# Kernel tuning notes

Measured on AMD Instinct MI355X. Metric: run time of the kernel, lower is better.

Reference implementation:

```python
import jax, jax.numpy as jnp
import numpy as np

KSIZE = 3  # module init kwarg


def setup_inputs() -> dict:
    key = jax.random.key(0)
    k1, k2, k3 = jax.random.split(key, 3)
    shape = (16, 3, 512, 512)  # [B, C, H, W]
    return {
        "sr": jax.random.normal(k1, shape, jnp.float32),
        "sr_ema": jax.random.normal(k2, shape, jnp.float32),
        "hr": jax.random.normal(k3, shape, jnp.float32),
    }


def _local_var(res, ksize):
    """Unbiased variance over a ksize x ksize sliding window with reflect pad.

    Matches torch: reflect-pad then unfold + var(unbiased=True). Implemented as a
    box-filter over sum and sum-of-squares (no ksize^2-larger unfold tensor).
    res: [B, 1, H, W] -> [B, 1, H, W]
    """
    pad = (ksize - 1) // 2
    rp = jnp.pad(res, ((0, 0), (0, 0), (pad, pad), (pad, pad)), mode="reflect")
    n = ksize * ksize
    win = (1, 1, ksize, ksize)
    strides = (1, 1, 1, 1)
    zero = jnp.zeros((), rp.dtype)
    s = jax.lax.reduce_window(rp, zero, jax.lax.add, win, strides, "VALID")
    sq = jax.lax.reduce_window(rp * rp, zero, jax.lax.add, win, strides, "VALID")
    # unbiased: (sum(x^2) - sum(x)^2/n) / (n-1)
    return (sq - s * s / n) / (n - 1)


def reference(sr, sr_ema, hr):
    # per-pixel channel-summed residuals, [B, 1, H, W]
    residual_ema = jnp.sum(jnp.abs(hr - sr_ema), axis=1, keepdims=True) / 255.0
    residual_sr = jnp.sum(jnp.abs(hr - sr), axis=1, keepdims=True) / 255.0

    r_det = jax.lax.stop_gradient(residual_sr)  # .clone().detach() in torch

    # patch-level weight: unbiased var over (C=1, H, W) per sample, ** (1/5)
    n_patch = r_det.shape[1] * r_det.shape[2] * r_det.shape[3]
    mean = jnp.mean(r_det, axis=(-1, -2, -3), keepdims=True)
    patch_var = jnp.sum((r_det - mean) ** 2, axis=(-1, -2, -3), keepdims=True) / (n_patch - 1)
    patch_w = patch_var ** 0.2  # [B,1,1,1]

    pixel_w = _local_var(r_det, KSIZE)  # [B,1,H,W]

    overall_w = patch_w * pixel_w
    overall_w = jnp.where(residual_sr < residual_ema, jnp.zeros((), overall_w.dtype), overall_w)

    # L1 loss (mean reduction) between weighted sr and weighted hr
    return jnp.mean(jnp.abs(overall_w * sr - overall_w * hr))
```

## Files before the change

kernel.cpp:

```cpp
#include <hip/hip_runtime.h>
#include <math.h>


#define BB 16
#define HH 512
#define WW 512
#define HW (HH * WW)
#define CHW (3 * HW)
#define BLOCKS_PER_BATCH 1024
#define NBLOCKS (BB * BLOCKS_PER_BATCH)

__global__ __launch_bounds__(256) void wl1_main(
    const float* __restrict__ sr, const float* __restrict__ srema,
    const float* __restrict__ hr,
    float* __restrict__ p_sum, float* __restrict__ p_sum2,
    float* __restrict__ p_loss) {
  __shared__ float rt[6][66];
  const int bid = blockIdx.x;
  const int b = bid >> 10;
  const int t = bid & 1023;
  const int h0 = (t >> 3) << 2;
  const int w0 = (t & 7) << 6;
  const int tid = threadIdx.x;
  const float* __restrict__ srb = sr + (size_t)b * CHW;
  const float* __restrict__ hrb = hr + (size_t)b * CHW;

  for (int idx = tid; idx < 6 * 66; idx += 256) {
    int row = idx / 66;
    int col = idx - row * 66;
    int gh = h0 - 1 + row;
    gh = gh < 0 ? -gh : gh;
    gh = gh >= HH ? 2 * HH - 2 - gh : gh;
    int gw = w0 - 1 + col;
    gw = gw < 0 ? -gw : gw;
    gw = gw >= WW ? 2 * WW - 2 - gw : gw;
    int base = gh * WW + gw;
    float s = fabsf(hrb[base] - srb[base]) +
              fabsf(hrb[base + HW] - srb[base + HW]) +
              fabsf(hrb[base + 2 * HW] - srb[base + 2 * HW]);
    rt[row][col] = s / 255.0f;
  }
  __syncthreads();

  const int lw = tid & 63, lh = tid >> 6;
  float s = 0.f, sq = 0.f;
#pragma unroll
  for (int dr = 0; dr < 3; ++dr)
#pragma unroll
    for (int dc = 0; dc < 3; ++dc) {
      float v = rt[lh + dr][lw + dc];
      s += v;
      sq += v * v;
    }
  float pvar = (sq - s * s / 9.0f) / 8.0f;
  float rc = rt[lh + 1][lw + 1];

  const int h = h0 + lh, w = w0 + lw;
  const int base = h * WW + w;
  const float* __restrict__ eb = srema + (size_t)b * CHW;
  float e = (fabsf(hrb[base] - eb[base]) +
             fabsf(hrb[base + HW] - eb[base + HW]) +
             fabsf(hrb[base + 2 * HW] - eb[base + 2 * HW])) /
            255.0f;

  float contrib = (rc < e) ? 0.0f : pvar * (255.0f * rc);

  float v1 = rc, v2 = rc * rc, v3 = contrib;
#pragma unroll
  for (int off = 32; off > 0; off >>= 1) {
    v1 += __shfl_down(v1, off, 64);
    v2 += __shfl_down(v2, off, 64);
    v3 += __shfl_down(v3, off, 64);
  }
  __shared__ float red[3][4];
  const int wave = tid >> 6, lane = tid & 63;
  if (lane == 0) {
    red[0][wave] = v1;
    red[1][wave] = v2;
    red[2][wave] = v3;
  }
  __syncthreads();
  if (tid == 0) {
    p_sum[bid] = red[0][0] + red[0][1] + red[0][2] + red[0][3];
    p_sum2[bid] = red[1][0] + red[1][1] + red[1][2] + red[1][3];
    p_loss[bid] = red[2][0] + red[2][1] + red[2][2] + red[2][3];
  }
}

__global__ __launch_bounds__(256) void wl1_batch(
    const float* __restrict__ p_sum, const float* __restrict__ p_sum2,
    const float* __restrict__ p_loss, double* __restrict__ lossb) {
  const int b = blockIdx.x, tid = threadIdx.x;
  double s = 0.0, s2 = 0.0, sl = 0.0;
  for (int k = tid; k < BLOCKS_PER_BATCH; k += 256) {
    int i = b * BLOCKS_PER_BATCH + k;
    s += (double)p_sum[i];
    s2 += (double)p_sum2[i];
    sl += (double)p_loss[i];
  }
#pragma unroll
  for (int off = 32; off > 0; off >>= 1) {
    s += __shfl_down(s, off, 64);
    s2 += __shfl_down(s2, off, 64);
    sl += __shfl_down(sl, off, 64);
  }
  __shared__ double red[3][4];
  const int wave = tid >> 6, lane = tid & 63;
  if (lane == 0) {
    red[0][wave] = s;
    red[1][wave] = s2;
    red[2][wave] = sl;
  }
  __syncthreads();
  if (tid == 0) {
    double S = red[0][0] + red[0][1] + red[0][2] + red[0][3];
    double S2 = red[1][0] + red[1][1] + red[1][2] + red[1][3];
    double SL = red[2][0] + red[2][1] + red[2][2] + red[2][3];
    const double n = (double)HW;
    double var = (S2 - S * S / n) / (n - 1.0);
    double pw = pow(var, 0.2);
    lossb[b] = pw * SL;
  }
}

__global__ void wl1_final(const double* __restrict__ lossb,
                          float* __restrict__ out) {
  const int tid = threadIdx.x;
  double v = (tid < BB) ? lossb[tid] : 0.0;
#pragma unroll
  for (int off = 32; off > 0; off >>= 1) v += __shfl_down(v, off, 64);
  if (tid == 0) out[0] = (float)(v / (double)(BB * 3 * HW));
}

extern "C" void kernel_launch(void* const* d_in, const int* in_sizes, int n_in,
                              void* d_out, int out_size, void* d_ws,
                              size_t ws_size, hipStream_t stream) {
  const float* sr = (const float*)d_in[0];
  const float* srema = (const float*)d_in[1];
  const float* hr = (const float*)d_in[2];
  float* out = (float*)d_out;

  float* p_sum = (float*)d_ws;
  float* p_sum2 = p_sum + NBLOCKS;
  float* p_loss = p_sum2 + NBLOCKS;
  double* lossb = (double*)((char*)d_ws + (size_t)3 * NBLOCKS * sizeof(float));

  wl1_main<<<NBLOCKS, 256, 0, stream>>>(sr, srema, hr, p_sum, p_sum2, p_loss);
  wl1_batch<<<BB, 256, 0, stream>>>(p_sum, p_sum2, p_loss, lossb);
  wl1_final<<<1, 64, 0, stream>>>(lossb, out);
}
```

Measured before the change: 164.7 us.

## Enlarge tiles to 16x256 with float4 loads and merge final reductions

Result: faster. 159.0 us (-3.4%).

```diff
diff --git a/kernel.cpp b/kernel.cpp
--- a/kernel.cpp
+++ b/kernel.cpp
@@ -7,65 +7,115 @@
 #define WW 512
 #define HW (HH * WW)
 #define CHW (3 * HW)
-#define BLOCKS_PER_BATCH 1024
-#define NBLOCKS (BB * BLOCKS_PER_BATCH)
+#define TILES_PER_BATCH 64
+#define NBLOCKS (BB * TILES_PER_BATCH)
+#define LDS_STRIDE 264
+
+__device__ __forceinline__ int reflect_h(int gh) {
+  gh = gh < 0 ? -gh : gh;
+  return gh >= HH ? 2 * HH - 2 - gh : gh;
+}
 
 __global__ __launch_bounds__(256) void wl1_main(
     const float* __restrict__ sr, const float* __restrict__ srema,
     const float* __restrict__ hr,
     float* __restrict__ p_sum, float* __restrict__ p_sum2,
     float* __restrict__ p_loss) {
-  __shared__ float rt[6][66];
+  __shared__ float rt[18][LDS_STRIDE];
   const int bid = blockIdx.x;
-  const int b = bid >> 10;
-  const int t = bid & 1023;
-  const int h0 = (t >> 3) << 2;
-  const int w0 = (t & 7) << 6;
+  const int b = bid >> 6;
+  const int t = bid & 63;
+  const int h0 = (t >> 1) << 4;
+  const int w0 = (t & 1) << 8;
   const int tid = threadIdx.x;
+  const int c4 = tid & 63;
+  const int rs = tid >> 6;
   const float* __restrict__ srb = sr + (size_t)b * CHW;
   const float* __restrict__ hrb = hr + (size_t)b * CHW;
+  const float* __restrict__ eb = srema + (size_t)b * CHW;
 
-  for (int idx = tid; idx < 6 * 66; idx += 256) {
-    int row = idx / 66;
-    int col = idx - row * 66;
-    int gh = h0 - 1 + row;
-    gh = gh < 0 ? -gh : gh;
-    gh = gh >= HH ? 2 * HH - 2 - gh : gh;
-    int gw = w0 - 1 + col;
-    gw = gw < 0 ? -gw : gw;
-    gw = gw >= WW ? 2 * WW - 2 - gw : gw;
+#pragma unroll
+  for (int it = 0; it < 5; ++it) {
+    int row = it * 4 + rs;
+    if (row < 18) {
+      int gh = reflect_h(h0 - 1 + row);
+      const float* hb = hrb + gh * WW + w0 + 4 * c4;
+      const float* sb = srb + gh * WW + w0 + 4 * c4;
+      float4 ha = *(const float4*)(hb);
+      float4 hbv = *(const float4*)(hb + HW);
+      float4 hc = *(const float4*)(hb + 2 * HW);
+      float4 sa = *(const float4*)(sb);
+      float4 sbv = *(const float4*)(sb + HW);
+      float4 sc = *(const float4*)(sb + 2 * HW);
+      float4 r4;
+      r4.x = (fabsf(ha.x - sa.x) + fabsf(hbv.x - sbv.x) + fabsf(hc.x - sc.x)) / 255.0f;
+      r4.y = (fabsf(ha.y - sa.y) + fabsf(hbv.y - sbv.y) + fabsf(hc.y - sc.y)) / 255.0f;
+      r4.z = (fabsf(ha.z - sa.z) + fabsf(hbv.z - sbv.z) + fabsf(hc.z - sc.z)) / 255.0f;
+      r4.w = (fabsf(ha.w - sa.w) + fabsf(hbv.w - sbv.w) + fabsf(hc.w - sc.w)) / 255.0f;
+      *(float4*)&rt[row][4 + 4 * c4] = r4;
+    }
+  }
+  if (tid < 36) {
+    int row = tid >> 1, side = tid & 1;
+    int gh = reflect_h(h0 - 1 + row);
+    int gw = side ? w0 + 256 : w0 - 1;
+    if (gw < 0) gw = 1;
+    if (gw > 511) gw = 1022 - gw;
     int base = gh * WW + gw;
-    float s = fabsf(hrb[base] - srb[base]) +
-              fabsf(hrb[base + HW] - srb[base + HW]) +
-              fabsf(hrb[base + 2 * HW] - srb[base + 2 * HW]);
-    rt[row][col] = s / 255.0f;
+    float v = (fabsf(hrb[base] - srb[base]) +
+               fabsf(hrb[base + HW] - srb[base + HW]) +
+               fabsf(hrb[base + 2 * HW] - srb[base + 2 * HW])) /
+              255.0f;
+    rt[row][side ? 260 : 3] = v;
   }
   __syncthreads();
 
-  const int lw = tid & 63, lh = tid >> 6;
-  float s = 0.f, sq = 0.f;
+  float v1 = 0.f, v2 = 0.f, v3 = 0.f;
+  const int row0 = rs * 4;
 #pragma unroll
-  for (int dr = 0; dr < 3; ++dr)
+  for (int rr = 0; rr < 4; ++rr) {
+    const int orow = row0 + rr;
+    float cs[6] = {0, 0, 0, 0, 0, 0}, cq[6] = {0, 0, 0, 0, 0, 0};
+    float center[4];
 #pragma unroll
-    for (int dc = 0; dc < 3; ++dc) {
-      float v = rt[lh + dr][lw + dc];
-      s += v;
-      sq += v * v;
+    for (int dr = 0; dr < 3; ++dr) {
+      const float* lp = &rt[orow + dr][4 * c4];
+      float4 a = *(const float4*)(lp);
+      float4 bq = *(const float4*)(lp + 4);
+      float4 cq4 = *(const float4*)(lp + 8);
+      float f3 = a.w, f4 = bq.x, f5 = bq.y, f6 = bq.z, f7 = bq.w, f8 = cq4.x;
+      cs[0] += f3; cq[0] += f3 * f3;
+      cs[1] += f4; cq[1] += f4 * f4;
+      cs[2] += f5; cq[2] += f5 * f5;
+      cs[3] += f6; cq[3] += f6 * f6;
+      cs[4] += f7; cq[4] += f7 * f7;
+      cs[5] += f8; cq[5] += f8 * f8;
+      if (dr == 1) { center[0] = f4; center[1] = f5; center[2] = f6; center[3] = f7; }
     }
-  float pvar = (sq - s * s / 9.0f) / 8.0f;
-  float rc = rt[lh + 1][lw + 1];
+    const int gbase = (h0 + orow) * WW + w0 + 4 * c4;
+    float4 ha = *(const float4*)(hrb + gbase);
+    float4 hb2 = *(const float4*)(hrb + gbase + HW);
+    float4 hc = *(const float4*)(hrb + gbase + 2 * HW);
+    float4 ea = *(const float4*)(eb + gbase);
+    float4 eb2 = *(const float4*)(eb + gbase + HW);
+    float4 ec = *(const float4*)(eb + gbase + 2 * HW);
+    float e4[4];
+    e4[0] = (fabsf(ha.x - ea.x) + fabsf(hb2.x - eb2.x) + fabsf(hc.x - ec.x)) / 255.0f;
+    e4[1] = (fabsf(ha.y - ea.y) + fabsf(hb2.y - eb2.y) + fabsf(hc.y - ec.y)) / 255.0f;
+    e4[2] = (fabsf(ha.z - ea.z) + fabsf(hb2.z - eb2.z) + fabsf(hc.z - ec.z)) / 255.0f;
+    e4[3] = (fabsf(ha.w - ea.w) + fabsf(hb2.w - eb2.w) + fabsf(hc.w - ec.w)) / 255.0f;
+#pragma unroll
+    for (int cc = 0; cc < 4; ++cc) {
+      float s = cs[cc] + cs[cc + 1] + cs[cc + 2];
+      float q = cq[cc] + cq[cc + 1] + cq[cc + 2];
+      float pvar = (q - s * s / 9.0f) / 8.0f;
+      float rc = center[cc];
+      v1 += rc;
+      v2 += rc * rc;
+      if (rc >= e4[cc]) v3 += pvar * (255.0f * rc);
+    }
+  }
 
-  const int h = h0 + lh, w = w0 + lw;
-  const int base = h * WW + w;
-  const float* __restrict__ eb = srema + (size_t)b * CHW;
-  float e = (fabsf(hrb[base] - eb[base]) +
-             fabsf(hrb[base + HW] - eb[base + HW]) +
-             fabsf(hrb[base + 2 * HW] - eb[base + 2 * HW])) /
-            255.0f;
-
-  float contrib = (rc < e) ? 0.0f : pvar * (255.0f * rc);
-
-  float v1 = rc, v2 = rc * rc, v3 = contrib;
 #pragma unroll
   for (int off = 32; off > 0; off >>= 1) {
     v1 += __shfl_down(v1, off, 64);
@@ -73,11 +123,10 @@
     v3 += __shfl_down(v3, off, 64);
   }
   __shared__ float red[3][4];
-  const int wave = tid >> 6, lane = tid & 63;
-  if (lane == 0) {
-    red[0][wave] = v1;
-    red[1][wave] = v2;
-    red[2][wave] = v3;
+  if (c4 == 0) {
+    red[0][rs] = v1;
+    red[1][rs] = v2;
+    red[2][rs] = v3;
   }
   __syncthreads();
   if (tid == 0) {
@@ -87,49 +136,32 @@
   }
 }
 
-__global__ __launch_bounds__(256) void wl1_batch(
+__global__ __launch_bounds__(1024) void wl1_reduce(
     const float* __restrict__ p_sum, const float* __restrict__ p_sum2,
-    const float* __restrict__ p_loss, double* __restrict__ lossb) {
-  const int b = blockIdx.x, tid = threadIdx.x;
-  double s = 0.0, s2 = 0.0, sl = 0.0;
-  for (int k = tid; k < BLOCKS_PER_BATCH; k += 256) {
-    int i = b * BLOCKS_PER_BATCH + k;
-    s += (double)p_sum[i];
-    s2 += (double)p_sum2[i];
-    sl += (double)p_loss[i];
-  }
+    const float* __restrict__ p_loss, float* __restrict__ out) {
+  const int tid = threadIdx.x;
+  const int b = tid >> 6, k = tid & 63;
+  const int i = b * TILES_PER_BATCH + k;
+  double s = (double)p_sum[i], s2 = (double)p_sum2[i], sl = (double)p_loss[i];
 #pragma unroll
   for (int off = 32; off > 0; off >>= 1) {
     s += __shfl_down(s, off, 64);
     s2 += __shfl_down(s2, off, 64);
     sl += __shfl_down(sl, off, 64);
   }
-  __shared__ double red[3][4];
-  const int wave = tid >> 6, lane = tid & 63;
-  if (lane == 0) {
-    red[0][wave] = s;
-    red[1][wave] = s2;
-    red[2][wave] = sl;
+  __shared__ double acc[BB];
+  if (k == 0) {
+    const double n = (double)HW;
+    double var = (s2 - s * s / n) / (n - 1.0);
+    acc[b] = pow(var, 0.2) * sl;
   }
   __syncthreads();
   if (tid == 0) {
-    double S = red[0][0] + red[0][1] + red[0][2] + red[0][3];
-    double S2 = red[1][0] + red[1][1] + red[1][2] + red[1][3];
-    double SL = red[2][0] + red[2][1] + red[2][2] + red[2][3];
-    const double n = (double)HW;
-    double var = (S2 - S * S / n) / (n - 1.0);
-    double pw = pow(var, 0.2);
-    lossb[b] = pw * SL;
+    double tot = 0.0;
+#pragma unroll
+    for (int j = 0; j < BB; ++j) tot += acc[j];
+    out[0] = (float)(tot / (double)((size_t)BB * CHW));
   }
-}
-
-__global__ void wl1_final(const double* __restrict__ lossb,
-                          float* __restrict__ out) {
-  const int tid = threadIdx.x;
-  double v = (tid < BB) ? lossb[tid] : 0.0;
-#pragma unroll
-  for (int off = 32; off > 0; off >>= 1) v += __shfl_down(v, off, 64);
-  if (tid == 0) out[0] = (float)(v / (double)(BB * 3 * HW));
 }
 
 extern "C" void kernel_launch(void* const* d_in, const int* in_sizes, int n_in,
@@ -143,9 +175,7 @@
   float* p_sum = (float*)d_ws;
   float* p_sum2 = p_sum + NBLOCKS;
   float* p_loss = p_sum2 + NBLOCKS;
-  double* lossb = (double*)((char*)d_ws + (size_t)3 * NBLOCKS * sizeof(float));
 
   wl1_main<<<NBLOCKS, 256, 0, stream>>>(sr, srema, hr, p_sum, p_sum2, p_loss);
-  wl1_batch<<<BB, 256, 0, stream>>>(p_sum, p_sum2, p_loss, lossb);
-  wl1_final<<<1, 64, 0, stream>>>(lossb, out);
+  wl1_reduce<<<1, 1024, 0, stream>>>(p_sum, p_sum2, p_loss, out);
 }
```
